# Performance work log

Measured on AMD Instinct MI355X. Metric: run time of the kernel, lower is better.

The kernel has to match this reference:

```python
import jax, jax.numpy as jnp
import numpy as np

N_NODES = 100000
IN_DIM = 256
HID = 128      # per-branch output_dim; concat -> 2*HID
N_CLASSES = 7
B, S0, S1 = 512, 25, 10
EPS = 1e-12


def setup_inputs() -> dict:
    key = jax.random.key(0)
    ks = jax.random.split(key, 16)
    d = {
        "ids": jax.random.randint(ks[0], (B,), 0, N_NODES),
        "ids1": jax.random.randint(ks[1], (B * S0,), 0, N_NODES),
        "ids2": jax.random.randint(ks[2], (B * S0 * S1,), 0, N_NODES),
        "feats": jax.random.normal(ks[3], (N_NODES, IN_DIM), dtype=jnp.float32),
        # layer-1 aggregator (input 256 -> concat 256)
        "W_x1": jax.random.normal(ks[4], (IN_DIM, HID), dtype=jnp.float32) * 0.05,
        "b_x1": jnp.zeros((HID,), dtype=jnp.float32),
        "W_n1": jax.random.normal(ks[5], (IN_DIM, HID), dtype=jnp.float32) * 0.05,
        "b_n1": jnp.zeros((HID,), dtype=jnp.float32),
        # layer-2 aggregator (input 256 -> concat 256)
        "W_x2": jax.random.normal(ks[6], (2 * HID, HID), dtype=jnp.float32) * 0.05,
        "b_x2": jnp.zeros((HID,), dtype=jnp.float32),
        "W_n2": jax.random.normal(ks[7], (2 * HID, HID), dtype=jnp.float32) * 0.05,
        "b_n2": jnp.zeros((HID,), dtype=jnp.float32),
        # final classifier
        "W_fc": jax.random.normal(ks[8], (2 * HID, N_CLASSES), dtype=jnp.float32) * 0.05,
        "b_fc": jnp.zeros((N_CLASSES,), dtype=jnp.float32),
    }
    return d


def _agg(x, neibs, Wx, bx, Wn, bn, act):
    # neibs: [len(x)*k, d] -> mean over k sampled neighbors per node
    m = neibs.reshape(x.shape[0], -1, neibs.shape[-1]).mean(axis=1)
    out = jnp.concatenate([x @ Wx + bx, m @ Wn + bn], axis=1)
    return act(out)


def reference(ids, ids1, ids2, feats,
              W_x1, b_x1, W_n1, b_n1,
              W_x2, b_x2, W_n2, b_n2,
              W_fc, b_fc):
    # multi-hop feature gathers (IdentityPrep)
    f0 = feats[ids]    # [B, d]
    f1 = feats[ids1]   # [B*S0, d]
    f2 = feats[ids2]   # [B*S0*S1, d]
    # aggregator layer 1 (relu), applied across consecutive hops
    h0 = _agg(f0, f1, W_x1, b_x1, W_n1, b_n1, jax.nn.relu)  # [B, 2*HID]
    h1 = _agg(f1, f2, W_x1, b_x1, W_n1, b_n1, jax.nn.relu)  # [B*S0, 2*HID]
    # aggregator layer 2 (no activation)
    g0 = _agg(h0, h1, W_x2, b_x2, W_n2, b_n2, lambda v: v)  # [B, 2*HID]
    # F.normalize(dim=1)
    out = g0 / jnp.maximum(jnp.linalg.norm(g0, axis=1, keepdims=True), EPS)
    return out @ W_fc + b_fc
```

## Files before the change

### kernel.cpp

```cpp
#include <hip/hip_runtime.h>
#include <hip/hip_bf16.h>


typedef __bf16 bf16x8 __attribute__((ext_vector_type(8)));
typedef __bf16 bf16x4 __attribute__((ext_vector_type(4)));
typedef float  f32x4  __attribute__((ext_vector_type(4)));

constexpr int IN    = 256;
constexpr int HIDC  = 128;
constexpr int ROWS1 = 512 * 25;

__global__ __launch_bounds__(256) void k_wprep(
    const float* __restrict__ Wx, const float* __restrict__ Wn,
    __bf16* __restrict__ WtH, __bf16* __restrict__ WtL)
{
    const int j = blockIdx.x;
    const int k = threadIdx.x;
    const float v = (j < HIDC) ? Wx[(size_t)k * HIDC + j]
                               : Wn[(size_t)k * HIDC + (j - HIDC)];
    const __bf16 h = (__bf16)v;
    const __bf16 l = (__bf16)(v - (float)h);
    const size_t o = (size_t)j * IN + k;
    WtH[o] = h;
    WtL[o] = l;
}

__global__ __launch_bounds__(512) void k_gath(
    const int* __restrict__ ids1, const int* __restrict__ ids2,
    const float* __restrict__ feats,
    __bf16* __restrict__ A0, __bf16* __restrict__ A1)
{
    const int r    = blockIdx.x * 8 + (threadIdx.x >> 6);
    const int lane = threadIdx.x & 63;
    const int base = r * 10;

    const float4 vx = ((const float4*)(feats + (size_t)ids1[r] * IN))[lane];
    float4 s = make_float4(0.f, 0.f, 0.f, 0.f);
    #pragma unroll
    for (int kk = 0; kk < 10; ++kk) {
        const float4 v = ((const float4*)(feats + (size_t)ids2[base + kk] * IN))[lane];
        s.x += v.x; s.y += v.y; s.z += v.z; s.w += v.w;
    }
    const bf16x4 a0 = {(__bf16)vx.x, (__bf16)vx.y, (__bf16)vx.z, (__bf16)vx.w};
    const bf16x4 a1 = {(__bf16)(s.x * 0.1f), (__bf16)(s.y * 0.1f),
                       (__bf16)(s.z * 0.1f), (__bf16)(s.w * 0.1f)};
    *(bf16x4*)&A0[(size_t)r * IN + lane * 4] = a0;
    *(bf16x4*)&A1[(size_t)r * IN + lane * 4] = a1;
}

__global__ __launch_bounds__(512) void k_gemm(
    const __bf16* __restrict__ A0, const __bf16* __restrict__ A1,
    const __bf16* __restrict__ WtH, const __bf16* __restrict__ WtL,
    const float* __restrict__ bx, const float* __restrict__ bn,
    __bf16* __restrict__ h1)
{
    __shared__ __bf16 As[64 * IN];
    const int tid   = threadIdx.x;
    const int strip = blockIdx.x >> 1;
    const int br    = blockIdx.x & 1;
    const int r0    = strip * 64;
    const __bf16* __restrict__ Ap = br ? A1 : A0;

    #pragma unroll
    for (int i = 0; i < 4; ++i) {
        const int idx = (i * 512 + tid) * 8;
        const bf16x8 v = *(const bf16x8*)&Ap[(size_t)r0 * IN + idx];
        const int row = idx >> 8;
        const int es  = idx ^ ((row & 7) << 3);
        *(bf16x8*)&As[es] = v;
    }
    __syncthreads();

    const int lane = tid & 63;
    const int w    = tid >> 6;
    const int l15  = lane & 15;
    const int lk   = lane >> 4;
    const int colL = w * 16 + l15;
    const int colG = br * HIDC + colL;
    const float bv = (br ? bn : bx)[colL];

    bf16x8 bh[8], bl[8];
    #pragma unroll
    for (int kb = 0; kb < 8; ++kb) {
        const size_t eb = (size_t)colG * IN + kb * 32 + lk * 8;
        bh[kb] = *(const bf16x8*)&WtH[eb];
        bl[kb] = *(const bf16x8*)&WtL[eb];
    }

    #pragma unroll
    for (int t = 0; t < 4; ++t) {
        const int rloc = t * 16 + l15;
        bf16x8 a[8];
        #pragma unroll
        for (int kb = 0; kb < 8; ++kb) {
            int ea = (rloc << 8) + kb * 32 + lk * 8;
            ea ^= (l15 & 7) << 3;
            a[kb] = *(const bf16x8*)&As[ea];
        }
        f32x4 acc = {0.f, 0.f, 0.f, 0.f};
        #pragma unroll
        for (int kb = 0; kb < 8; ++kb) {
            acc = __builtin_amdgcn_mfma_f32_16x16x32_bf16(a[kb], bh[kb], acc, 0, 0, 0);
            acc = __builtin_amdgcn_mfma_f32_16x16x32_bf16(a[kb], bl[kb], acc, 0, 0, 0);
        }
        #pragma unroll
        for (int q = 0; q < 4; ++q) {
            h1[(size_t)(r0 + t * 16 + lk * 4 + q) * IN + colG] =
                (__bf16)fmaxf(acc[q] + bv, 0.f);
        }
    }
}

__global__ __launch_bounds__(512) void k_out(
    const int* __restrict__ ids, const int* __restrict__ ids1,
    const float* __restrict__ feats,
    const __bf16* __restrict__ A0, const __bf16* __restrict__ h1,
    const float* __restrict__ Wx1, const float* __restrict__ bx1,
    const float* __restrict__ Wn1, const float* __restrict__ bn1,
    const float* __restrict__ Wx2, const float* __restrict__ bx2,
    const float* __restrict__ Wn2, const float* __restrict__ bn2,
    const float* __restrict__ Wfc, const float* __restrict__ bfc,
    float* __restrict__ out)
{
    __shared__ float x0[IN];
    __shared__ float m1[IN];
    __shared__ float mh[IN];
    __shared__ float h0[IN];
    __shared__ float g0[IN];
    __shared__ float partA[2][IN];
    __shared__ float partB[2][IN];
    __shared__ float red[8];
    __shared__ float fcred[7][4];
    const int i   = blockIdx.x;
    const int tid = threadIdx.x;
    const int c   = tid & 255;
    const int h   = tid >> 8;

    {
        float v1[13], v2[13];
        #pragma unroll
        for (int t = 0; t < 13; ++t) {
            const int kk = h * 13 + t;
            const int kc = kk < 25 ? kk : 24;
            const int r  = i * 25 + kc;
            v1[t] = (float)A0[(size_t)r * IN + c];
            v2[t] = (float)h1[(size_t)r * IN + c];
        }
        float s = 0.f, sh = 0.f;
        #pragma unroll
        for (int t = 0; t < 13; ++t) {
            const float msk = (h * 13 + t < 25) ? 1.f : 0.f;
            s  += msk * v1[t];
            sh += msk * v2[t];
        }
        if (h == 0) x0[c] = feats[(size_t)ids[i] * IN + c];
        partA[h][c] = s;
        partB[h][c] = sh;
    }
    __syncthreads();
    if (h == 0) m1[c] = (partA[0][c] + partA[1][c]) * 0.04f;
    else        mh[c] = (partB[0][c] + partB[1][c]) * 0.04f;
    __syncthreads();

    const int  jj = c & 127;
    const bool nb = (c >= 128);
    {
        const float* __restrict__ W = nb ? Wn1 : Wx1;
        const float* __restrict__ X = nb ? m1 : x0;
        float acc = 0.f;
        #pragma unroll 8
        for (int k = h * 128; k < h * 128 + 128; ++k)
            acc = fmaf(X[k], W[(size_t)k * HIDC + jj], acc);
        partA[h][c] = acc;
    }
    __syncthreads();
    if (h == 0)
        h0[c] = fmaxf(partA[0][c] + partA[1][c] + (nb ? bn1 : bx1)[jj], 0.f);
    __syncthreads();
    {
        const float* __restrict__ W = nb ? Wn2 : Wx2;
        const float* __restrict__ X = nb ? mh : h0;
        float acc = 0.f;
        #pragma unroll 8
        for (int k = h * 128; k < h * 128 + 128; ++k)
            acc = fmaf(X[k], W[(size_t)k * HIDC + jj], acc);
        partB[h][c] = acc;
    }
    __syncthreads();
    if (h == 0)
        g0[c] = partB[0][c] + partB[1][c] + (nb ? bn2 : bx2)[jj];
    __syncthreads();

    {
        const float gv = g0[c];
        float sq = gv * gv;
        #pragma unroll
        for (int off = 32; off > 0; off >>= 1) sq += __shfl_down(sq, off);
        if ((tid & 63) == 0) red[tid >> 6] = sq;
    }
    __syncthreads();
    const float total = (red[0] + red[1] + red[2] + red[3] +
                         red[4] + red[5] + red[6] + red[7]) * 0.5f;
    const float inv = 1.f / fmaxf(sqrtf(total), 1e-12f);
    const float p = g0[c] * inv;

    const int qbase = h * 4;
    const int qn    = h ? 3 : 4;
    for (int q = qbase; q < qbase + qn; ++q) {
        float t = p * Wfc[(size_t)c * 7 + q];
        #pragma unroll
        for (int off = 32; off > 0; off >>= 1) t += __shfl_down(t, off);
        if ((tid & 63) == 0) fcred[q][(tid >> 6) & 3] = t;
    }
    __syncthreads();
    if (tid < 7) {
        out[(size_t)i * 7 + tid] =
            fcred[tid][0] + fcred[tid][1] + fcred[tid][2] + fcred[tid][3] + bfc[tid];
    }
}

extern "C" void kernel_launch(void* const* d_in, const int* in_sizes, int n_in,
                              void* d_out, int out_size, void* d_ws, size_t ws_size,
                              hipStream_t stream) {
    const int*   ids   = (const int*)d_in[0];
    const int*   ids1  = (const int*)d_in[1];
    const int*   ids2  = (const int*)d_in[2];
    const float* feats = (const float*)d_in[3];
    const float* Wx1   = (const float*)d_in[4];
    const float* bx1   = (const float*)d_in[5];
    const float* Wn1   = (const float*)d_in[6];
    const float* bn1   = (const float*)d_in[7];
    const float* Wx2   = (const float*)d_in[8];
    const float* bx2   = (const float*)d_in[9];
    const float* Wn2   = (const float*)d_in[10];
    const float* bn2   = (const float*)d_in[11];
    const float* Wfc   = (const float*)d_in[12];
    const float* bfc   = (const float*)d_in[13];
    float* out = (float*)d_out;

    __bf16* A0  = (__bf16*)d_ws;
    __bf16* A1  = A0  + (size_t)ROWS1 * IN;
    __bf16* h1  = A1  + (size_t)ROWS1 * IN;
    __bf16* WtH = h1  + (size_t)ROWS1 * IN;
    __bf16* WtL = WtH + (size_t)IN * IN;

    k_wprep<<<256, 256, 0, stream>>>(Wx1, Wn1, WtH, WtL);
    k_gath<<<ROWS1 / 8, 512, 0, stream>>>(ids1, ids2, feats, A0, A1);
    k_gemm<<<400, 512, 0, stream>>>(A0, A1, WtH, WtL, bx1, bn1, h1);
    k_out<<<512, 512, 0, stream>>>(ids, ids1, feats, A0, h1,
                                   Wx1, bx1, Wn1, bn1,
                                   Wx2, bx2, Wn2, bn2,
                                   Wfc, bfc, out);
}
```

Baseline: 61.39 us.

## Pre-convert feature table to bf16 before gather; halve GEMM row tile

A new kernel converts the whole 100000x256 fp32 feature table to bf16 every call. The gather kernel then reads bf16 rows and accumulates them in fp32, so the random gathers move half the bytes. The layer-1 GEMM strip shrinks from 64 to 32 rows with twice as many blocks, for more parallelism. The full-table conversion reads 102MB and writes 51MB per call, far more than the roughly 16MB of fp32 rows the gather touches, so it adds a large streaming cost.

```diff
diff --git a/kernel.cpp b/kernel.cpp
--- a/kernel.cpp
+++ b/kernel.cpp
@@ -8,7 +8,22 @@
 
 constexpr int IN    = 256;
 constexpr int HIDC  = 128;
+constexpr int NNODE = 100000;
 constexpr int ROWS1 = 512 * 25;
+
+__global__ __launch_bounds__(512) void k_conv(
+    const float* __restrict__ feats, __bf16* __restrict__ fbf)
+{
+    const size_t e = ((size_t)blockIdx.x * 512 + threadIdx.x) * 16;
+    const float4* src = (const float4*)(feats + e);
+    const float4 v0 = src[0], v1 = src[1], v2 = src[2], v3 = src[3];
+    const bf16x8 o0 = {(__bf16)v0.x, (__bf16)v0.y, (__bf16)v0.z, (__bf16)v0.w,
+                       (__bf16)v1.x, (__bf16)v1.y, (__bf16)v1.z, (__bf16)v1.w};
+    const bf16x8 o1 = {(__bf16)v2.x, (__bf16)v2.y, (__bf16)v2.z, (__bf16)v2.w,
+                       (__bf16)v3.x, (__bf16)v3.y, (__bf16)v3.z, (__bf16)v3.w};
+    *(bf16x8*)(fbf + e)     = o0;
+    *(bf16x8*)(fbf + e + 8) = o1;
+}
 
 __global__ __launch_bounds__(256) void k_wprep(
     const float* __restrict__ Wx, const float* __restrict__ Wn,
@@ -27,24 +42,23 @@
 
 __global__ __launch_bounds__(512) void k_gath(
     const int* __restrict__ ids1, const int* __restrict__ ids2,
-    const float* __restrict__ feats,
+    const __bf16* __restrict__ fbf,
     __bf16* __restrict__ A0, __bf16* __restrict__ A1)
 {
     const int r    = blockIdx.x * 8 + (threadIdx.x >> 6);
     const int lane = threadIdx.x & 63;
     const int base = r * 10;
 
-    const float4 vx = ((const float4*)(feats + (size_t)ids1[r] * IN))[lane];
-    float4 s = make_float4(0.f, 0.f, 0.f, 0.f);
+    const bf16x4 vx = *(const bf16x4*)&fbf[(size_t)ids1[r] * IN + lane * 4];
+    float s0 = 0.f, s1 = 0.f, s2 = 0.f, s3 = 0.f;
     #pragma unroll
     for (int kk = 0; kk < 10; ++kk) {
-        const float4 v = ((const float4*)(feats + (size_t)ids2[base + kk] * IN))[lane];
-        s.x += v.x; s.y += v.y; s.z += v.z; s.w += v.w;
-    }
-    const bf16x4 a0 = {(__bf16)vx.x, (__bf16)vx.y, (__bf16)vx.z, (__bf16)vx.w};
-    const bf16x4 a1 = {(__bf16)(s.x * 0.1f), (__bf16)(s.y * 0.1f),
-                       (__bf16)(s.z * 0.1f), (__bf16)(s.w * 0.1f)};
-    *(bf16x4*)&A0[(size_t)r * IN + lane * 4] = a0;
+        const bf16x4 v = *(const bf16x4*)&fbf[(size_t)ids2[base + kk] * IN + lane * 4];
+        s0 += (float)v.x; s1 += (float)v.y; s2 += (float)v.z; s3 += (float)v.w;
+    }
+    const bf16x4 a1 = {(__bf16)(s0 * 0.1f), (__bf16)(s1 * 0.1f),
+                       (__bf16)(s2 * 0.1f), (__bf16)(s3 * 0.1f)};
+    *(bf16x4*)&A0[(size_t)r * IN + lane * 4] = vx;
     *(bf16x4*)&A1[(size_t)r * IN + lane * 4] = a1;
 }
 
@@ -54,15 +68,15 @@
     const float* __restrict__ bx, const float* __restrict__ bn,
     __bf16* __restrict__ h1)
 {
-    __shared__ __bf16 As[64 * IN];
+    __shared__ __bf16 As[32 * IN];
     const int tid   = threadIdx.x;
     const int strip = blockIdx.x >> 1;
     const int br    = blockIdx.x & 1;
-    const int r0    = strip * 64;
+    const int r0    = strip * 32;
     const __bf16* __restrict__ Ap = br ? A1 : A0;
 
     #pragma unroll
-    for (int i = 0; i < 4; ++i) {
+    for (int i = 0; i < 2; ++i) {
         const int idx = (i * 512 + tid) * 8;
         const bf16x8 v = *(const bf16x8*)&Ap[(size_t)r0 * IN + idx];
         const int row = idx >> 8;
@@ -88,7 +102,7 @@
     }
 
     #pragma unroll
-    for (int t = 0; t < 4; ++t) {
+    for (int t = 0; t < 2; ++t) {
         const int rloc = t * 16 + l15;
         bf16x8 a[8];
         #pragma unroll
@@ -238,15 +252,17 @@
     const float* bfc   = (const float*)d_in[13];
     float* out = (float*)d_out;
 
-    __bf16* A0  = (__bf16*)d_ws;
+    __bf16* fbf = (__bf16*)d_ws;
+    __bf16* A0  = fbf + (size_t)NNODE * IN;
     __bf16* A1  = A0  + (size_t)ROWS1 * IN;
     __bf16* h1  = A1  + (size_t)ROWS1 * IN;
     __bf16* WtH = h1  + (size_t)ROWS1 * IN;
     __bf16* WtL = WtH + (size_t)IN * IN;
 
+    k_conv<<<(NNODE * IN) / (512 * 16), 512, 0, stream>>>(feats, fbf);
     k_wprep<<<256, 256, 0, stream>>>(Wx1, Wn1, WtH, WtL);
-    k_gath<<<ROWS1 / 8, 512, 0, stream>>>(ids1, ids2, feats, A0, A1);
-    k_gemm<<<400, 512, 0, stream>>>(A0, A1, WtH, WtL, bx1, bn1, h1);
+    k_gath<<<ROWS1 / 8, 512, 0, stream>>>(ids1, ids2, fbf, A0, A1);
+    k_gemm<<<800, 512, 0, stream>>>(A0, A1, WtH, WtL, bx1, bn1, h1);
     k_out<<<512, 512, 0, stream>>>(ids, ids1, feats, A0, h1,
                                    Wx1, bx1, Wn1, bn1,
                                    Wx2, bx2, Wn2, bn2,
```

After: 77.90 us. 1.27x slower.
